# Optimization experiments

Hardware: AMD Instinct MI355X
Metric: run time of the kernel (lower is better)

The kernel has to match this reference:

```python
import jax, jax.numpy as jnp
import numpy as np

N_NODES = 65536
N_EDGES = 1048576
D_FEAT = 64
UNITS = 64


def setup_inputs() -> dict:
    key = jax.random.key(0)
    k1, k2, k3, k4, k5 = jax.random.split(key, 5)
    nodes = jax.random.normal(k1, (N_NODES, D_FEAT), dtype=jnp.float32)
    edge_vals = jax.random.uniform(k2, (N_EDGES,), dtype=jnp.float32)
    kernel = jax.random.normal(k3, (D_FEAT, UNITS), dtype=jnp.float32) * (1.0 / np.sqrt(D_FEAT))
    src_idx = jax.random.randint(k4, (N_EDGES,), 0, N_NODES, dtype=jnp.int32)
    dst_idx = jnp.sort(jax.random.randint(k5, (N_EDGES,), 0, N_NODES, dtype=jnp.int32))
    return {"nodes": nodes, "edge_vals": edge_vals, "kernel": kernel,
            "src_idx": src_idx, "dst_idx": dst_idx}


def reference(nodes, edge_vals, kernel, src_idx, dst_idx):
    # sparse_dense_matmul(A, X): for each edge (dst, src, w): agg[dst] += w * X[src]
    msgs = edge_vals[:, None] * nodes[src_idx]          # [E, d]
    agg = jax.ops.segment_sum(msgs, dst_idx, num_segments=nodes.shape[0])  # [N, d]
    # dense projection (activation is None -> linear)
    return agg @ kernel                                  # [N, units]
```

## Files before the change

kernel.cpp:

```cpp
#include <hip/hip_runtime.h>
#include <hip/hip_bf16.h>


constexpr int D = 64;
constexpr int EPW = 128;

__global__ __launch_bounds__(256) void zero_kernel(float4* __restrict__ p, int n4) {
    int i = blockIdx.x * blockDim.x + threadIdx.x;
    int stride = gridDim.x * blockDim.x;
    for (; i < n4; i += stride) p[i] = make_float4(0.f, 0.f, 0.f, 0.f);
}

__global__ __launch_bounds__(256) void gemm_rows(const float* __restrict__ nodes,
                                                 const float* __restrict__ Km,
                                                 __hip_bfloat16* __restrict__ P,
                                                 int n_nodes) {
    const int lane = threadIdx.x & 63;
    float kcol[D];
    #pragma unroll
    for (int d = 0; d < D; ++d) kcol[d] = Km[d * D + lane];

    const int wid = (blockIdx.x * blockDim.x + threadIdx.x) >> 6;
    const int urow0 = __builtin_amdgcn_readfirstlane(wid * 8);

    #pragma unroll 1
    for (int i = 0; i < 8; ++i) {
        const int row = urow0 + i;
        if (row >= n_nodes) return;
        const float4* rp = (const float4*)(nodes + (long)row * D);
        float4 a[16];
        #pragma unroll
        for (int q = 0; q < 16; ++q) a[q] = rp[q];
        const float* af = (const float*)a;
        float acc0 = 0.f, acc1 = 0.f, acc2 = 0.f, acc3 = 0.f;
        #pragma unroll
        for (int d = 0; d < D; d += 4) {
            acc0 = fmaf(af[d + 0], kcol[d + 0], acc0);
            acc1 = fmaf(af[d + 1], kcol[d + 1], acc1);
            acc2 = fmaf(af[d + 2], kcol[d + 2], acc2);
            acc3 = fmaf(af[d + 3], kcol[d + 3], acc3);
        }
        const float acc = (acc0 + acc1) + (acc2 + acc3);
        __hip_bfloat16 b = __float2bfloat16(acc);
        P[(long)row * D + lane] = b;
    }
}

template <typename T>
__device__ __forceinline__ float load_feat(const T* P, long idx);
template <>
__device__ __forceinline__ float load_feat<__hip_bfloat16>(const __hip_bfloat16* P, long idx) {
    return __bfloat162float(P[idx]);
}
template <>
__device__ __forceinline__ float load_feat<float>(const float* P, long idx) { return P[idx]; }

template <typename T>
__global__ __launch_bounds__(256) void scatter_sorted(
    const T* __restrict__ P, const float* __restrict__ evals,
    const int* __restrict__ src, const int* __restrict__ dst,
    float* __restrict__ out, int n_edges)
{
    const int lane = threadIdx.x & 63;
    const int wid  = blockIdx.x * (blockDim.x >> 6) + (threadIdx.x >> 6);
    const long base = (long)wid * EPW;
    if (base >= n_edges) return;
    const int ubase = __builtin_amdgcn_readfirstlane((int)base);

    const int first = dst[ubase];
    int prev = first;
    float acc = 0.f;

    if ((long)ubase + EPW <= (long)n_edges) {
        #pragma unroll 1
        for (int i0 = 0; i0 < EPW; i0 += 16) {
            const int4*   sp = (const int4*)  (src   + ubase + i0);
            const int4*   dp = (const int4*)  (dst   + ubase + i0);
            const float4* wp = (const float4*)(evals + ubase + i0);
            const int4   sv0 = sp[0], sv1 = sp[1], sv2 = sp[2], sv3 = sp[3];
            const int4   dv0 = dp[0], dv1 = dp[1], dv2 = dp[2], dv3 = dp[3];
            const float4 wv0 = wp[0], wv1 = wp[1], wv2 = wp[2], wv3 = wp[3];

            const int svs[16] = {sv0.x, sv0.y, sv0.z, sv0.w, sv1.x, sv1.y, sv1.z, sv1.w,
                                 sv2.x, sv2.y, sv2.z, sv2.w, sv3.x, sv3.y, sv3.z, sv3.w};
            float v[16];
            #pragma unroll
            for (int k = 0; k < 16; ++k) {
                const T* prow = P + (long)svs[k] * D;
                v[k] = load_feat<T>(prow, lane);
            }

            const int   dvs[16] = {dv0.x, dv0.y, dv0.z, dv0.w, dv1.x, dv1.y, dv1.z, dv1.w,
                                   dv2.x, dv2.y, dv2.z, dv2.w, dv3.x, dv3.y, dv3.z, dv3.w};
            const float wvs[16] = {wv0.x, wv0.y, wv0.z, wv0.w, wv1.x, wv1.y, wv1.z, wv1.w,
                                   wv2.x, wv2.y, wv2.z, wv2.w, wv3.x, wv3.y, wv3.z, wv3.w};
            #pragma unroll
            for (int k = 0; k < 16; ++k) {
                if (dvs[k] != prev) {
                    float* o = &out[(long)prev * D + lane];
                    if (prev == first) atomicAdd(o, acc);
                    else               *o = acc;
                    acc = 0.f;
                    prev = dvs[k];
                }
                acc = fmaf(wvs[k], v[k], acc);
            }
        }
    } else {
        for (long e = ubase; e < n_edges; ++e) {
            int s = src[e], dc = dst[e]; float w = evals[e];
            float v = load_feat<T>(P, (long)s * D + lane);
            if (dc != prev) {
                float* o = &out[(long)prev * D + lane];
                if (prev == first) atomicAdd(o, acc);
                else               *o = acc;
                acc = 0.f;
                prev = dc;
            }
            acc = fmaf(w, v, acc);
        }
    }
    atomicAdd(&out[(long)prev * D + lane], acc);
}

__global__ __launch_bounds__(256) void project_inplace(float* __restrict__ out,
                                                       const float* __restrict__ Km, int n_nodes) {
    __shared__ float Ks[D * D];
    const int t = threadIdx.x;
    for (int i = t; i < D * D; i += 256) Ks[i] = Km[i];
    __syncthreads();
    const int lane = t & 63;
    const int n = blockIdx.x * 4 + (t >> 6);
    if (n >= n_nodes) return;
    float* row = out + (long)n * D;
    const float rv = row[lane];
    float acc = 0.f;
    #pragma unroll
    for (int d = 0; d < D; ++d) acc = fmaf(__shfl(rv, d), Ks[d * D + lane], acc);
    row[lane] = acc;
}

extern "C" void kernel_launch(void* const* d_in, const int* in_sizes, int n_in,
                              void* d_out, int out_size, void* d_ws, size_t ws_size,
                              hipStream_t stream) {
    const float* nodes = (const float*)d_in[0];
    const float* evals = (const float*)d_in[1];
    const float* Km    = (const float*)d_in[2];
    const int*   src   = (const int*)d_in[3];
    const int*   dst   = (const int*)d_in[4];
    float* out = (float*)d_out;

    const int n_nodes = in_sizes[0] / D;
    const int n_edges = in_sizes[1];
    const int n_waves = (n_edges + EPW - 1) / EPW;

    zero_kernel<<<2048, 256, 0, stream>>>((float4*)out, out_size / 4);

    const size_t need = (size_t)n_nodes * D * sizeof(__hip_bfloat16);
    if (ws_size >= need) {
        __hip_bfloat16* P = (__hip_bfloat16*)d_ws;
        const int gw = (n_nodes + 7) / 8;
        gemm_rows<<<(gw + 3) / 4, 256, 0, stream>>>(nodes, Km, P, n_nodes);
        scatter_sorted<__hip_bfloat16><<<(n_waves + 3) / 4, 256, 0, stream>>>(
            P, evals, src, dst, out, n_edges);
    } else {
        scatter_sorted<float><<<(n_waves + 3) / 4, 256, 0, stream>>>(
            nodes, evals, src, dst, out, n_edges);
        project_inplace<<<(n_nodes + 3) / 4, 256, 0, stream>>>(out, Km, n_nodes);
    }
}
```

Baseline: 116.6 us.

## Replace edge-parallel atomic scatter with CSR row-pointer per-node gather aggregation

Builds a CSR row-pointer array from the sorted destination indices. The aggregation then runs one wave per node, gathering that node's edges and writing its output row directly. This removes the output zeroing pass and the atomics at segment boundaries. In exchange it adds a row-pointer build kernel, and because edges per node vary, the per-node loop lengths are uneven and some aligned loads fetch edges that fall outside the node's range and are masked off.

After: 128.8 us. 10.5% more time.

```diff
diff --git a/kernel.cpp b/kernel.cpp
--- a/kernel.cpp
+++ b/kernel.cpp
@@ -46,18 +46,75 @@
     }
 }
 
+__global__ __launch_bounds__(256) void build_rowptr(const int* __restrict__ dst,
+                                                    int* __restrict__ rp,
+                                                    int n_edges, int n_nodes) {
+    int e = blockIdx.x * blockDim.x + threadIdx.x;
+    const int stride = gridDim.x * blockDim.x;
+    for (; e < n_edges; e += stride) {
+        const int d = dst[e];
+        const int pd = (e == 0) ? -1 : dst[e - 1];
+        if (d != pd)
+            for (int n = pd + 1; n <= d; ++n) rp[n] = e;
+        if (e == n_edges - 1)
+            for (int n = d + 1; n <= n_nodes; ++n) rp[n] = n_edges;
+    }
+}
+
+__global__ __launch_bounds__(256) void agg_nodes(const __hip_bfloat16* __restrict__ P,
+                                                 const float* __restrict__ evals,
+                                                 const int* __restrict__ src,
+                                                 const int* __restrict__ rp,
+                                                 float* __restrict__ out,
+                                                 int n_nodes, int n_edges) {
+    const int lane = threadIdx.x & 63;
+    const int n = (blockIdx.x * blockDim.x + threadIdx.x) >> 6;
+    if (n >= n_nodes) return;
+    const int lo = __builtin_amdgcn_readfirstlane(rp[n]);
+    const int hi = __builtin_amdgcn_readfirstlane(rp[n + 1]);
+
+    float acc = 0.f;
+    int e0 = lo & ~3;
+    #pragma unroll 1
+    while (e0 < hi) {
+        if (e0 + 8 <= n_edges) {
+            const int4   s0 = *(const int4*)(src + e0);
+            const int4   s1 = *(const int4*)(src + e0 + 4);
+            const float4 w0 = *(const float4*)(evals + e0);
+            const float4 w1 = *(const float4*)(evals + e0 + 4);
+            const int   sv[8]   = {s0.x, s0.y, s0.z, s0.w, s1.x, s1.y, s1.z, s1.w};
+            const float wraw[8] = {w0.x, w0.y, w0.z, w0.w, w1.x, w1.y, w1.z, w1.w};
+            float v[8];
+            #pragma unroll
+            for (int j = 0; j < 8; ++j) {
+                const int sj = __builtin_amdgcn_readfirstlane(sv[j]);
+                v[j] = __bfloat162float(P[(long)sj * D + lane]);
+            }
+            #pragma unroll
+            for (int j = 0; j < 8; ++j) {
+                const int e = e0 + j;
+                const float w = (e >= lo && e < hi) ? wraw[j] : 0.f;
+                acc = fmaf(w, v[j], acc);
+            }
+            e0 += 8;
+        } else {
+            for (int e = (e0 > lo ? e0 : lo); e < hi; ++e) {
+                const int sj = __builtin_amdgcn_readfirstlane(src[e]);
+                acc = fmaf(evals[e], __bfloat162float(P[(long)sj * D + lane]), acc);
+            }
+            break;
+        }
+    }
+    out[(long)n * D + lane] = acc;
+}
+
 template <typename T>
 __device__ __forceinline__ float load_feat(const T* P, long idx);
 template <>
-__device__ __forceinline__ float load_feat<__hip_bfloat16>(const __hip_bfloat16* P, long idx) {
-    return __bfloat162float(P[idx]);
-}
-template <>
 __device__ __forceinline__ float load_feat<float>(const float* P, long idx) { return P[idx]; }
 
-template <typename T>
-__global__ __launch_bounds__(256) void scatter_sorted(
-    const T* __restrict__ P, const float* __restrict__ evals,
+__global__ __launch_bounds__(256) void scatter_sorted_f32(
+    const float* __restrict__ P, const float* __restrict__ evals,
     const int* __restrict__ src, const int* __restrict__ dst,
     float* __restrict__ out, int n_edges)
 {
@@ -71,54 +128,19 @@
     int prev = first;
     float acc = 0.f;
 
-    if ((long)ubase + EPW <= (long)n_edges) {
-        #pragma unroll 1
-        for (int i0 = 0; i0 < EPW; i0 += 16) {
-            const int4*   sp = (const int4*)  (src   + ubase + i0);
-            const int4*   dp = (const int4*)  (dst   + ubase + i0);
-            const float4* wp = (const float4*)(evals + ubase + i0);
-            const int4   sv0 = sp[0], sv1 = sp[1], sv2 = sp[2], sv3 = sp[3];
-            const int4   dv0 = dp[0], dv1 = dp[1], dv2 = dp[2], dv3 = dp[3];
-            const float4 wv0 = wp[0], wv1 = wp[1], wv2 = wp[2], wv3 = wp[3];
-
-            const int svs[16] = {sv0.x, sv0.y, sv0.z, sv0.w, sv1.x, sv1.y, sv1.z, sv1.w,
-                                 sv2.x, sv2.y, sv2.z, sv2.w, sv3.x, sv3.y, sv3.z, sv3.w};
-            float v[16];
-            #pragma unroll
-            for (int k = 0; k < 16; ++k) {
-                const T* prow = P + (long)svs[k] * D;
-                v[k] = load_feat<T>(prow, lane);
-            }
-
-            const int   dvs[16] = {dv0.x, dv0.y, dv0.z, dv0.w, dv1.x, dv1.y, dv1.z, dv1.w,
-                                   dv2.x, dv2.y, dv2.z, dv2.w, dv3.x, dv3.y, dv3.z, dv3.w};
-            const float wvs[16] = {wv0.x, wv0.y, wv0.z, wv0.w, wv1.x, wv1.y, wv1.z, wv1.w,
-                                   wv2.x, wv2.y, wv2.z, wv2.w, wv3.x, wv3.y, wv3.z, wv3.w};
-            #pragma unroll
-            for (int k = 0; k < 16; ++k) {
-                if (dvs[k] != prev) {
-                    float* o = &out[(long)prev * D + lane];
-                    if (prev == first) atomicAdd(o, acc);
-                    else               *o = acc;
-                    acc = 0.f;
-                    prev = dvs[k];
-                }
-                acc = fmaf(wvs[k], v[k], acc);
-            }
+    #pragma unroll 1
+    for (int i0 = 0; i0 < EPW && ubase + i0 < n_edges; i0 += 1) {
+        const long e = ubase + i0;
+        int s = src[e], dc = dst[e]; float w = evals[e];
+        float v = P[(long)s * D + lane];
+        if (dc != prev) {
+            float* o = &out[(long)prev * D + lane];
+            if (prev == first) atomicAdd(o, acc);
+            else               *o = acc;
+            acc = 0.f;
+            prev = dc;
         }
-    } else {
-        for (long e = ubase; e < n_edges; ++e) {
-            int s = src[e], dc = dst[e]; float w = evals[e];
-            float v = load_feat<T>(P, (long)s * D + lane);
-            if (dc != prev) {
-                float* o = &out[(long)prev * D + lane];
-                if (prev == first) atomicAdd(o, acc);
-                else               *o = acc;
-                acc = 0.f;
-                prev = dc;
-            }
-            acc = fmaf(w, v, acc);
-        }
+        acc = fmaf(w, v, acc);
     }
     atomicAdd(&out[(long)prev * D + lane], acc);
 }
@@ -152,19 +174,23 @@
 
     const int n_nodes = in_sizes[0] / D;
     const int n_edges = in_sizes[1];
-    const int n_waves = (n_edges + EPW - 1) / EPW;
 
-    zero_kernel<<<2048, 256, 0, stream>>>((float4*)out, out_size / 4);
+    const size_t p_bytes  = (size_t)n_nodes * D * sizeof(__hip_bfloat16);
+    const size_t rp_bytes = (size_t)(n_nodes + 1) * sizeof(int);
 
-    const size_t need = (size_t)n_nodes * D * sizeof(__hip_bfloat16);
-    if (ws_size >= need) {
+    if (ws_size >= p_bytes + rp_bytes) {
         __hip_bfloat16* P = (__hip_bfloat16*)d_ws;
+        int* rp = (int*)((char*)d_ws + p_bytes);
+
+        build_rowptr<<<2048, 256, 0, stream>>>(dst, rp, n_edges, n_nodes);
         const int gw = (n_nodes + 7) / 8;
         gemm_rows<<<(gw + 3) / 4, 256, 0, stream>>>(nodes, Km, P, n_nodes);
-        scatter_sorted<__hip_bfloat16><<<(n_waves + 3) / 4, 256, 0, stream>>>(
-            P, evals, src, dst, out, n_edges);
+        agg_nodes<<<(n_nodes + 3) / 4, 256, 0, stream>>>(P, evals, src, rp, out,
+                                                         n_nodes, n_edges);
     } else {
-        scatter_sorted<float><<<(n_waves + 3) / 4, 256, 0, stream>>>(
+        zero_kernel<<<2048, 256, 0, stream>>>((float4*)out, out_size / 4);
+        const int n_waves = (n_edges + EPW - 1) / EPW;
+        scatter_sorted_f32<<<(n_waves + 3) / 4, 256, 0, stream>>>(
             nodes, evals, src, dst, out, n_edges);
         project_inplace<<<(n_nodes + 3) / 4, 256, 0, stream>>>(out, Km, n_nodes);
     }
```

## Gather four edges per wave with 8-byte bf16 loads and ballot-based segment flushing

Applied to the files above, without the earlier changes.

The scatter kernel now splits each wave into four 16-lane groups. Each group gathers a different edge row as 8-byte packed bf16 loads, so one wave instruction fetches four rows instead of one. Run boundaries are found with a ballot over dst loaded one edge per lane, and partial sums are reduced across groups with xor shuffles before the store or atomic. This should raise memory-level parallelism and cut load instruction count, at the price of cross-lane shuffles and extra masked FMAs on segment boundaries. The fallback path is simplified to plain per-edge atomics.

Result: slower. 122.5 us (+5.0%).

```diff
diff --git a/kernel.cpp b/kernel.cpp
--- a/kernel.cpp
+++ b/kernel.cpp
@@ -13,7 +13,7 @@
 
 __global__ __launch_bounds__(256) void gemm_rows(const float* __restrict__ nodes,
                                                  const float* __restrict__ Km,
-                                                 __hip_bfloat16* __restrict__ P,
+                                                 ushort* __restrict__ P,
                                                  int n_nodes) {
     const int lane = threadIdx.x & 63;
     float kcol[D];
@@ -42,22 +42,109 @@
         }
         const float acc = (acc0 + acc1) + (acc2 + acc3);
         __hip_bfloat16 b = __float2bfloat16(acc);
-        P[(long)row * D + lane] = b;
+        P[(long)row * D + lane] = *(ushort*)&b;
     }
 }
 
-template <typename T>
-__device__ __forceinline__ float load_feat(const T* P, long idx);
-template <>
-__device__ __forceinline__ float load_feat<__hip_bfloat16>(const __hip_bfloat16* P, long idx) {
-    return __bfloat162float(P[idx]);
-}
-template <>
-__device__ __forceinline__ float load_feat<float>(const float* P, long idx) { return P[idx]; }
-
-template <typename T>
-__global__ __launch_bounds__(256) void scatter_sorted(
-    const T* __restrict__ P, const float* __restrict__ evals,
+__device__ __forceinline__ float sel4(int g, float4 a) {
+    float v01 = (g & 1) ? a.y : a.x;
+    float v23 = (g & 1) ? a.w : a.z;
+    return (g & 2) ? v23 : v01;
+}
+
+__device__ __forceinline__ void flush_run(float* __restrict__ out, int prev,
+                                          bool use_atomic, float4& acc,
+                                          int f, int g) {
+    float4 a = acc;
+    a.x += __shfl_xor(a.x, 16); a.x += __shfl_xor(a.x, 32);
+    a.y += __shfl_xor(a.y, 16); a.y += __shfl_xor(a.y, 32);
+    a.z += __shfl_xor(a.z, 16); a.z += __shfl_xor(a.z, 32);
+    a.w += __shfl_xor(a.w, 16); a.w += __shfl_xor(a.w, 32);
+    const float val = sel4(g, a);
+    float* p = out + (long)prev * D + f * 4 + g;
+    if (use_atomic) atomicAdd(p, val);
+    else            *p = val;
+    acc = make_float4(0.f, 0.f, 0.f, 0.f);
+}
+
+__global__ __launch_bounds__(256) void scatter_packed(
+    const ushort* __restrict__ P, const float* __restrict__ evals,
+    const int* __restrict__ src, const int* __restrict__ dst,
+    float* __restrict__ out, int n_edges)
+{
+    const int lane = threadIdx.x & 63;
+    const int g = lane >> 4;
+    const int f = lane & 15;
+    const int wid = blockIdx.x * (blockDim.x >> 6) + (threadIdx.x >> 6);
+    const long base = (long)wid * EPW;
+    if (base >= n_edges) return;
+
+    if (base + EPW <= n_edges) {
+        const int first = dst[base];
+        int prev = first;
+        float4 acc = make_float4(0.f, 0.f, 0.f, 0.f);
+
+        #pragma unroll 1
+        for (int i0 = 0; i0 < EPW; i0 += 64) {
+            const long eb = base + i0;
+            const int   sl = src[eb + lane];
+            const int   dl = dst[eb + lane];
+            const float wl = evals[eb + lane];
+
+            const int dpv = __shfl_up(dl, 1);
+            const bool bnd = (lane == 0) ? (dl != prev) : (dl != dpv);
+            const unsigned long long bmask = __ballot(bnd);
+
+            uint2 v[16];
+            #pragma unroll
+            for (int u = 0; u < 16; ++u) {
+                const int row = __shfl(sl, 4 * u + g);
+                v[u] = *(const uint2*)(P + (long)row * D + f * 4);
+            }
+
+            #pragma unroll
+            for (int u = 0; u < 16; ++u) {
+                const float wme = __shfl(wl, 4 * u + g);
+                float4 pv;
+                pv.x = __uint_as_float(v[u].x << 16);
+                pv.y = __uint_as_float(v[u].x & 0xffff0000u);
+                pv.z = __uint_as_float(v[u].y << 16);
+                pv.w = __uint_as_float(v[u].y & 0xffff0000u);
+                const unsigned bb = (unsigned)((bmask >> (4 * u)) & 0xFull);
+                if (bb == 0u) {
+                    acc.x = fmaf(wme, pv.x, acc.x);
+                    acc.y = fmaf(wme, pv.y, acc.y);
+                    acc.z = fmaf(wme, pv.z, acc.z);
+                    acc.w = fmaf(wme, pv.w, acc.w);
+                } else {
+                    #pragma unroll
+                    for (int k = 0; k < 4; ++k) {
+                        if ((bb >> k) & 1u) {
+                            flush_run(out, prev, prev == first, acc, f, g);
+                            prev = __shfl(dl, 4 * u + k);
+                        }
+                        const float wk = (g == k) ? wme : 0.f;
+                        acc.x = fmaf(wk, pv.x, acc.x);
+                        acc.y = fmaf(wk, pv.y, acc.y);
+                        acc.z = fmaf(wk, pv.z, acc.z);
+                        acc.w = fmaf(wk, pv.w, acc.w);
+                    }
+                }
+            }
+        }
+        flush_run(out, prev, true, acc, f, g);
+    } else {
+        for (long e = base; e < n_edges; ++e) {
+            const int s = src[e];
+            const float w = evals[e];
+            const float pvf = __uint_as_float(((unsigned)P[(long)s * D + lane]) << 16);
+            atomicAdd(&out[(long)dst[e] * D + lane], w * pvf);
+        }
+    }
+}
+
+__global__ __launch_bounds__(256) void scatter_simple_f32(
+    const float* __restrict__ nodes, const float* __restrict__ evals,
     const int* __restrict__ src, const int* __restrict__ dst,
     float* __restrict__ out, int n_edges)
 {
@@ -65,62 +152,9 @@
     const int wid  = blockIdx.x * (blockDim.x >> 6) + (threadIdx.x >> 6);
     const long base = (long)wid * EPW;
     if (base >= n_edges) return;
-    const int ubase = __builtin_amdgcn_readfirstlane((int)base);
-
-    const int first = dst[ubase];
-    int prev = first;
-    float acc = 0.f;
-
-    if ((long)ubase + EPW <= (long)n_edges) {
-        #pragma unroll 1
-        for (int i0 = 0; i0 < EPW; i0 += 16) {
-            const int4*   sp = (const int4*)  (src   + ubase + i0);
-            const int4*   dp = (const int4*)  (dst   + ubase + i0);
-            const float4* wp = (const float4*)(evals + ubase + i0);
-            const int4   sv0 = sp[0], sv1 = sp[1], sv2 = sp[2], sv3 = sp[3];
-            const int4   dv0 = dp[0], dv1 = dp[1], dv2 = dp[2], dv3 = dp[3];
-            const float4 wv0 = wp[0], wv1 = wp[1], wv2 = wp[2], wv3 = wp[3];
-
-            const int svs[16] = {sv0.x, sv0.y, sv0.z, sv0.w, sv1.x, sv1.y, sv1.z, sv1.w,
-                                 sv2.x, sv2.y, sv2.z, sv2.w, sv3.x, sv3.y, sv3.z, sv3.w};
-            float v[16];
-            #pragma unroll
-            for (int k = 0; k < 16; ++k) {
-                const T* prow = P + (long)svs[k] * D;
-                v[k] = load_feat<T>(prow, lane);
-            }
-
-            const int   dvs[16] = {dv0.x, dv0.y, dv0.z, dv0.w, dv1.x, dv1.y, dv1.z, dv1.w,
-                                   dv2.x, dv2.y, dv2.z, dv2.w, dv3.x, dv3.y, dv3.z, dv3.w};
-            const float wvs[16] = {wv0.x, wv0.y, wv0.z, wv0.w, wv1.x, wv1.y, wv1.z, wv1.w,
-                                   wv2.x, wv2.y, wv2.z, wv2.w, wv3.x, wv3.y, wv3.z, wv3.w};
-            #pragma unroll
-            for (int k = 0; k < 16; ++k) {
-                if (dvs[k] != prev) {
-                    float* o = &out[(long)prev * D + lane];
-                    if (prev == first) atomicAdd(o, acc);
-                    else               *o = acc;
-                    acc = 0.f;
-                    prev = dvs[k];
-                }
-                acc = fmaf(wvs[k], v[k], acc);
-            }
-        }
-    } else {
-        for (long e = ubase; e < n_edges; ++e) {
-            int s = src[e], dc = dst[e]; float w = evals[e];
-            float v = load_feat<T>(P, (long)s * D + lane);
-            if (dc != prev) {
-                float* o = &out[(long)prev * D + lane];
-                if (prev == first) atomicAdd(o, acc);
-                else               *o = acc;
-                acc = 0.f;
-                prev = dc;
-            }
-            acc = fmaf(w, v, acc);
-        }
-    }
-    atomicAdd(&out[(long)prev * D + lane], acc);
+    long end = base + EPW; if (end > n_edges) end = n_edges;
+    for (long e = base; e < end; ++e)
+        atomicAdd(&out[(long)dst[e] * D + lane], evals[e] * nodes[(long)src[e] * D + lane]);
 }
 
 __global__ __launch_bounds__(256) void project_inplace(float* __restrict__ out,
@@ -156,15 +190,15 @@
 
     zero_kernel<<<2048, 256, 0, stream>>>((float4*)out, out_size / 4);
 
-    const size_t need = (size_t)n_nodes * D * sizeof(__hip_bfloat16);
-    if (ws_size >= need) {
-        __hip_bfloat16* P = (__hip_bfloat16*)d_ws;
+    const size_t p_bytes = (size_t)n_nodes * D * sizeof(ushort);
+    if (ws_size >= p_bytes) {
+        ushort* P = (ushort*)d_ws;
         const int gw = (n_nodes + 7) / 8;
         gemm_rows<<<(gw + 3) / 4, 256, 0, stream>>>(nodes, Km, P, n_nodes);
-        scatter_sorted<__hip_bfloat16><<<(n_waves + 3) / 4, 256, 0, stream>>>(
+        scatter_packed<<<(n_waves + 3) / 4, 256, 0, stream>>>(
             P, evals, src, dst, out, n_edges);
     } else {
-        scatter_sorted<float><<<(n_waves + 3) / 4, 256, 0, stream>>>(
+        scatter_simple_f32<<<(n_waves + 3) / 4, 256, 0, stream>>>(
             nodes, evals, src, dst, out, n_edges);
         project_inplace<<<(n_nodes + 3) / 4, 256, 0, stream>>>(out, Km, n_nodes);
     }
```

## Issue all 64 gathers per wave up front with lane-loaded indices and ballot segment mask

Applied to the files above, without the earlier changes.

The sorted scatter kernel now handles 64 edges per wave. Each lane loads one edge's src, dst and weight, and a ballot finds the segment boundaries. The kernel then issues all 64 bf16 row gathers back to back before accumulating, with per-edge values broadcast through readlane. The aim is much deeper memory-level parallelism and fewer scalar index loads, at the cost of higher register pressure (64 raw values per lane) and about twice as many boundary atomics from the smaller edge chunks. The fallback float path is also simplified to plain per-edge atomics.

Measured after the change: 115.4 us. About the same (-1.0%).

```diff
diff --git a/kernel.cpp b/kernel.cpp
--- a/kernel.cpp
+++ b/kernel.cpp
@@ -3,7 +3,7 @@
 
 
 constexpr int D = 64;
-constexpr int EPW = 128;
+constexpr int EPW = 64;
 
 __global__ __launch_bounds__(256) void zero_kernel(float4* __restrict__ p, int n4) {
     int i = blockIdx.x * blockDim.x + threadIdx.x;
@@ -13,7 +13,7 @@
 
 __global__ __launch_bounds__(256) void gemm_rows(const float* __restrict__ nodes,
                                                  const float* __restrict__ Km,
-                                                 __hip_bfloat16* __restrict__ P,
+                                                 ushort* __restrict__ P,
                                                  int n_nodes) {
     const int lane = threadIdx.x & 63;
     float kcol[D];
@@ -42,22 +42,12 @@
         }
         const float acc = (acc0 + acc1) + (acc2 + acc3);
         __hip_bfloat16 b = __float2bfloat16(acc);
-        P[(long)row * D + lane] = b;
+        P[(long)row * D + lane] = *(ushort*)&b;
     }
 }
 
-template <typename T>
-__device__ __forceinline__ float load_feat(const T* P, long idx);
-template <>
-__device__ __forceinline__ float load_feat<__hip_bfloat16>(const __hip_bfloat16* P, long idx) {
-    return __bfloat162float(P[idx]);
-}
-template <>
-__device__ __forceinline__ float load_feat<float>(const float* P, long idx) { return P[idx]; }
-
-template <typename T>
-__global__ __launch_bounds__(256) void scatter_sorted(
-    const T* __restrict__ P, const float* __restrict__ evals,
+__global__ __launch_bounds__(256) void scatter_deep(
+    const ushort* __restrict__ P, const float* __restrict__ evals,
     const int* __restrict__ src, const int* __restrict__ dst,
     float* __restrict__ out, int n_edges)
 {
@@ -65,62 +55,60 @@
     const int wid  = blockIdx.x * (blockDim.x >> 6) + (threadIdx.x >> 6);
     const long base = (long)wid * EPW;
     if (base >= n_edges) return;
-    const int ubase = __builtin_amdgcn_readfirstlane((int)base);
 
-    const int first = dst[ubase];
-    int prev = first;
-    float acc = 0.f;
+    if (base + EPW <= n_edges) {
+        const int   svl = src[base + lane];
+        const int   dvl = dst[base + lane];
+        const float wvl = evals[base + lane];
 
-    if ((long)ubase + EPW <= (long)n_edges) {
-        #pragma unroll 1
-        for (int i0 = 0; i0 < EPW; i0 += 16) {
-            const int4*   sp = (const int4*)  (src   + ubase + i0);
-            const int4*   dp = (const int4*)  (dst   + ubase + i0);
-            const float4* wp = (const float4*)(evals + ubase + i0);
-            const int4   sv0 = sp[0], sv1 = sp[1], sv2 = sp[2], sv3 = sp[3];
-            const int4   dv0 = dp[0], dv1 = dp[1], dv2 = dp[2], dv3 = dp[3];
-            const float4 wv0 = wp[0], wv1 = wp[1], wv2 = wp[2], wv3 = wp[3];
+        const int dprev = __shfl_up(dvl, 1);
+        const unsigned long long bmask = __ballot(lane > 0 && dvl != dprev);
 
-            const int svs[16] = {sv0.x, sv0.y, sv0.z, sv0.w, sv1.x, sv1.y, sv1.z, sv1.w,
-                                 sv2.x, sv2.y, sv2.z, sv2.w, sv3.x, sv3.y, sv3.z, sv3.w};
-            float v[16];
-            #pragma unroll
-            for (int k = 0; k < 16; ++k) {
-                const T* prow = P + (long)svs[k] * D;
-                v[k] = load_feat<T>(prow, lane);
-            }
+        unsigned raw[EPW];
+        #pragma unroll
+        for (int j = 0; j < EPW; ++j) {
+            const int row = __builtin_amdgcn_readlane(svl, j);
+            raw[j] = P[(long)row * D + lane];
+        }
 
-            const int   dvs[16] = {dv0.x, dv0.y, dv0.z, dv0.w, dv1.x, dv1.y, dv1.z, dv1.w,
-                                   dv2.x, dv2.y, dv2.z, dv2.w, dv3.x, dv3.y, dv3.z, dv3.w};
-            const float wvs[16] = {wv0.x, wv0.y, wv0.z, wv0.w, wv1.x, wv1.y, wv1.z, wv1.w,
-                                   wv2.x, wv2.y, wv2.z, wv2.w, wv3.x, wv3.y, wv3.z, wv3.w};
-            #pragma unroll
-            for (int k = 0; k < 16; ++k) {
-                if (dvs[k] != prev) {
-                    float* o = &out[(long)prev * D + lane];
-                    if (prev == first) atomicAdd(o, acc);
-                    else               *o = acc;
-                    acc = 0.f;
-                    prev = dvs[k];
-                }
-                acc = fmaf(wvs[k], v[k], acc);
-            }
-        }
-    } else {
-        for (long e = ubase; e < n_edges; ++e) {
-            int s = src[e], dc = dst[e]; float w = evals[e];
-            float v = load_feat<T>(P, (long)s * D + lane);
-            if (dc != prev) {
+        const int first = __builtin_amdgcn_readlane(dvl, 0);
+        int prev = first;
+        float acc = 0.f;
+        #pragma unroll
+        for (int j = 0; j < EPW; ++j) {
+            if ((bmask >> j) & 1ull) {
                 float* o = &out[(long)prev * D + lane];
                 if (prev == first) atomicAdd(o, acc);
                 else               *o = acc;
                 acc = 0.f;
-                prev = dc;
+                prev = __builtin_amdgcn_readlane(dvl, j);
             }
-            acc = fmaf(w, v, acc);
+            const float w =
+                __uint_as_float(__builtin_amdgcn_readlane(__float_as_uint(wvl), j));
+            acc = fmaf(w, __uint_as_float(raw[j] << 16), acc);
+        }
+        atomicAdd(&out[(long)prev * D + lane], acc);
+    } else {
+        for (long e = base; e < n_edges; ++e) {
+            const float pv =
+                __uint_as_float(((unsigned)P[(long)src[e] * D + lane]) << 16);
+            atomicAdd(&out[(long)dst[e] * D + lane], evals[e] * pv);
         }
     }
-    atomicAdd(&out[(long)prev * D + lane], acc);
+}
+
+__global__ __launch_bounds__(256) void scatter_simple_f32(
+    const float* __restrict__ nodes, const float* __restrict__ evals,
+    const int* __restrict__ src, const int* __restrict__ dst,
+    float* __restrict__ out, int n_edges)
+{
+    const int lane = threadIdx.x & 63;
+    const int wid  = blockIdx.x * (blockDim.x >> 6) + (threadIdx.x >> 6);
+    const long base = (long)wid * 128;
+    if (base >= n_edges) return;
+    long end = base + 128; if (end > n_edges) end = n_edges;
+    for (long e = base; e < end; ++e)
+        atomicAdd(&out[(long)dst[e] * D + lane], evals[e] * nodes[(long)src[e] * D + lane]);
 }
 
 __global__ __launch_bounds__(256) void project_inplace(float* __restrict__ out,
@@ -156,15 +144,16 @@
 
     zero_kernel<<<2048, 256, 0, stream>>>((float4*)out, out_size / 4);
 
-    const size_t need = (size_t)n_nodes * D * sizeof(__hip_bfloat16);
-    if (ws_size >= need) {
-        __hip_bfloat16* P = (__hip_bfloat16*)d_ws;
+    const size_t p_bytes = (size_t)n_nodes * D * sizeof(ushort);
+    if (ws_size >= p_bytes) {
+        ushort* P = (ushort*)d_ws;
         const int gw = (n_nodes + 7) / 8;
         gemm_rows<<<(gw + 3) / 4, 256, 0, stream>>>(nodes, Km, P, n_nodes);
-        scatter_sorted<__hip_bfloat16><<<(n_waves + 3) / 4, 256, 0, stream>>>(
+        scatter_deep<<<(n_waves + 3) / 4, 256, 0, stream>>>(
             P, evals, src, dst, out, n_edges);
     } else {
-        scatter_sorted<float><<<(n_waves + 3) / 4, 256, 0, stream>>>(
+        const int fw = (n_edges + 127) / 128;
+        scatter_simple_f32<<<(fw + 3) / 4, 256, 0, stream>>>(
             nodes, evals, src, dst, out, n_edges);
         project_inplace<<<(n_nodes + 3) / 4, 256, 0, stream>>>(out, Km, n_nodes);
     }
```
